# Kernel optimization log

Measured on AMD Instinct MI355X. Metric: run time of the kernel, lower is better.

The kernel has to match this reference:

```python
import jax, jax.numpy as jnp
import numpy as np

B, S, V, D, H, C, NH = 8, 512, 32000, 768, 768, 9, 8
DH = D // NH


def setup_inputs() -> dict:
    key = jax.random.key(0)
    ks = list(jax.random.split(key, 24))
    it = iter(ks)

    def w(shape, s=0.02):
        return jax.random.normal(next(it), shape, jnp.float32) * s

    return {
        "input_ids": jax.random.randint(next(it), (B, S), 0, V, dtype=jnp.int32),
        "labels": jax.random.randint(next(it), (B, S), 0, C, dtype=jnp.int32),
        "emb_table": w((V, D), 1.0),
        "hw_Wh": w((D, D)),
        "hw_bh": jnp.zeros((D,), jnp.float32),
        "hw_Wt": w((D, D)),
        "hw_bt": jnp.zeros((D,), jnp.float32),
        "in_proj_w": w((3 * D, D)),
        "in_proj_b": jnp.zeros((3 * D,), jnp.float32),
        "out_proj_w": w((D, D)),
        "out_proj_b": jnp.zeros((D,), jnp.float32),
        "lstm0_Wih": w((2, 4 * H, D)),
        "lstm0_Whh": w((2, 4 * H, H)),
        "lstm0_b": jnp.zeros((2, 4 * H), jnp.float32),
        "lstm1_Wih": w((2, 4 * H, 2 * H)),
        "lstm1_Whh": w((2, 4 * H, H)),
        "lstm1_b": jnp.zeros((2, 4 * H), jnp.float32),
        "fc_W": w((C, 2 * H)),
        "fc_b": jnp.zeros((C,), jnp.float32),
        "crf_start": w((C,), 0.1),
        "crf_end": w((C,), 0.1),
        "crf_trans": w((C, C), 0.1),
    }


def _lstm_dir(x, Wih, Whh, b, reverse):
    # x: [B,S,in] -> outputs [B,S,H]; PyTorch gate order i,f,g,o
    xt = x.transpose(1, 0, 2)  # [S,B,in]
    h0 = jnp.zeros((x.shape[0], H), x.dtype)

    def step(carry, xt_):
        h, c = carry
        g = xt_ @ Wih.T + h @ Whh.T + b
        i, f, gg, o = jnp.split(g, 4, axis=-1)
        c = jax.nn.sigmoid(f) * c + jax.nn.sigmoid(i) * jnp.tanh(gg)
        h = jax.nn.sigmoid(o) * jnp.tanh(c)
        return (h, c), h

    _, hs = jax.lax.scan(step, (h0, h0), xt, reverse=reverse)
    return hs.transpose(1, 0, 2)


def _bilstm_layer(x, Wih, Whh, b):
    fwd = _lstm_dir(x, Wih[0], Whh[0], b[0], False)
    bwd = _lstm_dir(x, Wih[1], Whh[1], b[1], True)
    return jnp.concatenate([fwd, bwd], axis=-1)


def _emissions(input_ids, emb_table, hw_Wh, hw_bh, hw_Wt, hw_bt,
               in_proj_w, in_proj_b, out_proj_w, out_proj_b,
               lstm0_Wih, lstm0_Whh, lstm0_b, lstm1_Wih, lstm1_Whh, lstm1_b,
               fc_W, fc_b):
    x = emb_table[input_ids]  # [B,S,D]
    # Highway (1 layer, relu)
    hh = jax.nn.relu(x @ hw_Wh.T + hw_bh)
    t = jax.nn.sigmoid(x @ hw_Wt.T + hw_bt)
    x = t * hh + (1.0 - t) * x
    # Multi-head self-attention
    qkv = x @ in_proj_w.T + in_proj_b
    q, k, v = jnp.split(qkv, 3, axis=-1)
    hd = lambda a: a.reshape(B, S, NH, DH).transpose(0, 2, 1, 3)  # [B,NH,S,DH]
    q, k, v = hd(q), hd(k), hd(v)
    att = jax.nn.softmax(jnp.einsum('bhqd,bhkd->bhqk', q, k) / np.float32(np.sqrt(DH)), axis=-1)
    o = jnp.einsum('bhqk,bhkd->bhqd', att, v).transpose(0, 2, 1, 3).reshape(B, S, D)
    x = o @ out_proj_w.T + out_proj_b
    # 2-layer BiLSTM (inference: dropout off)
    x = _bilstm_layer(x, lstm0_Wih, lstm0_Whh, lstm0_b)
    x = _bilstm_layer(x, lstm1_Wih, lstm1_Whh, lstm1_b)
    return x @ fc_W.T + fc_b  # [B,S,C]


def _crf_nll(emissions, tags, crf_start, crf_end, crf_trans):
    # full mask (labels==-100 replaced by 0 before mask built), reduction='sum'
    em_t = emissions.transpose(1, 0, 2)  # [S,B,C]
    num = crf_start[tags[:, 0]] + crf_end[tags[:, -1]]
    num = num + jnp.take_along_axis(emissions, tags[..., None], axis=-1)[..., 0].sum(-1)
    num = num + crf_trans[tags[:, :-1], tags[:, 1:]].sum(-1)
    a0 = crf_start + em_t[0]  # [B,C]

    def fstep(a, em):
        a = jax.scipy.special.logsumexp(a[:, :, None] + crf_trans[None], axis=1) + em
        return a, None

    aT, _ = jax.lax.scan(fstep, a0, em_t[1:])
    logZ = jax.scipy.special.logsumexp(aT + crf_end, axis=-1)
    return -(num - logZ).sum()


def _viterbi(emissions, crf_start, crf_end, crf_trans):
    em_t = emissions.transpose(1, 0, 2)  # [S,B,C]
    s0 = crf_start + em_t[0]

    def vstep(s, em):
        sc = s[:, :, None] + crf_trans[None]  # [B,C_prev,C_next]
        return jnp.max(sc, axis=1) + em, jnp.argmax(sc, axis=1)

    sT, bps = jax.lax.scan(vstep, s0, em_t[1:])  # bps: [S-1,B,C]
    last = jnp.argmax(sT + crf_end, axis=-1)  # [B]

    def bstep(tag, bp):
        prev = jnp.take_along_axis(bp, tag[:, None], axis=1)[:, 0]
        return prev, prev

    _, path = jax.lax.scan(bstep, last, bps, reverse=True)  # [S-1,B]
    return jnp.concatenate([path, last[None]], axis=0).transpose(1, 0)  # [B,S]


def reference(input_ids, labels, emb_table, hw_Wh, hw_bh, hw_Wt, hw_bt,
              in_proj_w, in_proj_b, out_proj_w, out_proj_b,
              lstm0_Wih, lstm0_Whh, lstm0_b, lstm1_Wih, lstm1_Whh, lstm1_b,
              fc_W, fc_b, crf_start, crf_end, crf_trans):
    emissions = _emissions(input_ids, emb_table, hw_Wh, hw_bh, hw_Wt, hw_bt,
                           in_proj_w, in_proj_b, out_proj_w, out_proj_b,
                           lstm0_Wih, lstm0_Whh, lstm0_b,
                           lstm1_Wih, lstm1_Whh, lstm1_b, fc_W, fc_b)
    loss = _crf_nll(emissions, labels, crf_start, crf_end, crf_trans)
    decode = _viterbi(emissions, crf_start, crf_end, crf_trans)
    return loss, decode
```

## Files before the change

### kernel.cpp

```cpp
#include <hip/hip_runtime.h>
#include <hip/hip_bf16.h>
#include <cstdint>

#define B_   8
#define S_   512
#define D_   768
#define C_   9
#define BS_  4096

typedef unsigned long long u64;
typedef unsigned short ushort_t;
typedef short bf16x8 __attribute__((ext_vector_type(8)));
typedef float f32x4 __attribute__((ext_vector_type(4)));

__global__ __launch_bounds__(192) void k_embed(const int* __restrict__ ids,
                                               const float* __restrict__ emb,
                                               float* __restrict__ x) {
  int row = blockIdx.x;
  int id = ids[row];
  const float4* src = (const float4*)(emb + (size_t)id * D_);
  float4* dst = (float4*)(x + (size_t)row * D_);
  dst[threadIdx.x] = src[threadIdx.x];
}

#define GIDX(k, m) ((k)*144 + (m) + (((m) >> 5) << 2))

__global__ __launch_bounds__(256) void k_gemm(const float* __restrict__ A,
                                              const float* __restrict__ W,
                                              const float* __restrict__ bias,
                                              float* __restrict__ C,
                                              int M, int N, int K, int act, int mode) {
  __shared__ float As[2304];
  __shared__ float Bs[2304];
  int nwg = gridDim.x * gridDim.y;
  int lin = blockIdx.y * gridDim.x + blockIdx.x;
  int cpx = nwg >> 3;
  int swz = (lin & 7) * cpx + (lin >> 3);
  int bxs = swz % gridDim.x, bys = swz / gridDim.x;
  int bm0 = bys * 128, bn0 = bxs * 128;
  int tid = threadIdx.x;
  int tm = tid >> 4, tn = tid & 15;
  float acc[8][8];
#pragma unroll
  for (int i = 0; i < 8; ++i)
#pragma unroll
    for (int j = 0; j < 8; ++j) acc[i][j] = 0.f;

  for (int k0 = 0; k0 < K; k0 += 16) {
    __syncthreads();
#pragma unroll
    for (int j = 0; j < 2; ++j) {
      int f4 = tid + j * 256;
      int r = f4 >> 2;
      int kq = (f4 & 3) * 4;
      float4 va = *(const float4*)(A + (size_t)(bm0 + r) * K + k0 + kq);
      As[GIDX(kq + 0, r)] = va.x; As[GIDX(kq + 1, r)] = va.y;
      As[GIDX(kq + 2, r)] = va.z; As[GIDX(kq + 3, r)] = va.w;
      float4 vb = *(const float4*)(W + (size_t)(bn0 + r) * K + k0 + kq);
      Bs[GIDX(kq + 0, r)] = vb.x; Bs[GIDX(kq + 1, r)] = vb.y;
      Bs[GIDX(kq + 2, r)] = vb.z; Bs[GIDX(kq + 3, r)] = vb.w;
    }
    __syncthreads();
#pragma unroll
    for (int kk = 0; kk < 16; ++kk) {
      float a[8], b[8];
      *(float4*)&a[0] = *(const float4*)&As[GIDX(kk, tm * 8)];
      *(float4*)&a[4] = *(const float4*)&As[GIDX(kk, tm * 8 + 4)];
      *(float4*)&b[0] = *(const float4*)&Bs[GIDX(kk, tn * 8)];
      *(float4*)&b[4] = *(const float4*)&Bs[GIDX(kk, tn * 8 + 4)];
#pragma unroll
      for (int i = 0; i < 8; ++i)
#pragma unroll
        for (int j = 0; j < 8; ++j) acc[i][j] += a[i] * b[j];
    }
  }

  float bv[8];
#pragma unroll
  for (int j = 0; j < 8; ++j) bv[j] = bias[bn0 + tn * 8 + j];
#pragma unroll
  for (int i = 0; i < 8; ++i) {
    int row = bm0 + tm * 8 + i;
    float o[8];
#pragma unroll
    for (int j = 0; j < 8; ++j) {
      float v = acc[i][j] + bv[j];
      if (act == 1) v = fmaxf(v, 0.f);
      else if (act == 2) v = 1.f / (1.f + expf(-v));
      o[j] = v;
    }
    if (mode == 0) {
      float* cp = C + (size_t)row * N + bn0 + tn * 8;
      *(float4*)cp = make_float4(o[0], o[1], o[2], o[3]);
      *(float4*)(cp + 4) = make_float4(o[4], o[5], o[6], o[7]);
    } else {
      int bb = row >> 9, t = row & 511;
#pragma unroll
      for (int j = 0; j < 8; ++j) {
        unsigned n = bn0 + tn * 8 + j;
        unsigned dir = n / 3072u;
        unsigned n2 = n - dir * 3072u;
        unsigned g = n2 / 768u;
        unsigned rem = n2 - g * 768u;
        unsigned grp = rem >> 3, u = rem & 7;
        C[(((size_t)(dir * 512 + t) * 96 + grp) << 8) + u * 32 + g * 8 + bb] = o[j];
      }
    }
  }
}

__device__ inline ushort_t f2bf_bits(float x) {
  __hip_bfloat16 h = __float2bfloat16(x);
  return __builtin_bit_cast(ushort_t, h);
}
__device__ inline float bf2f(ushort_t b) {
  return __bfloat162float(__builtin_bit_cast(__hip_bfloat16, b));
}

__global__ __launch_bounds__(256) void k_cvt(const float* __restrict__ src,
                                             ushort_t* __restrict__ dst,
                                             int K, int total4, int mode) {
  int kq4 = K >> 2;
  for (int idx = blockIdx.x * 256 + threadIdx.x; idx < total4; idx += gridDim.x * 256) {
    int m = idx / kq4;
    int kq = (idx - m * kq4) * 4;
    float4 v = *(const float4*)(src + (size_t)m * K + kq);
    ushort4 hi, lo;
    hi.x = f2bf_bits(v.x); lo.x = f2bf_bits(v.x - bf2f(hi.x));
    hi.y = f2bf_bits(v.y); lo.y = f2bf_bits(v.y - bf2f(hi.y));
    hi.z = f2bf_bits(v.z); lo.z = f2bf_bits(v.z - bf2f(hi.z));
    hi.w = f2bf_bits(v.w); lo.w = f2bf_bits(v.w - bf2f(hi.w));
    ushort_t* base = dst + (size_t)m * 3 * K + kq;
    *(ushort4*)(base)         = hi;
    *(ushort4*)(base + K)     = mode ? hi : lo;
    *(ushort4*)(base + 2 * K) = mode ? lo : hi;
  }
}

__global__ __launch_bounds__(256) void k_gates16(const ushort_t* __restrict__ A,
                                                 const ushort_t* __restrict__ W,
                                                 const float* __restrict__ bias,
                                                 float* __restrict__ C,
                                                 int Kp) {
  __shared__ ushort_t Asb[128 * 64];
  __shared__ ushort_t Bsb[128 * 64];
  int nwg = gridDim.x * gridDim.y;
  int lin = blockIdx.y * gridDim.x + blockIdx.x;
  int cpx = nwg >> 3;
  int swz = (lin & 7) * cpx + (lin >> 3);
  int bn0 = (swz % gridDim.x) * 128, bm0 = (swz / gridDim.x) * 128;
  int tid = threadIdx.x;
  int w = tid >> 6, lane = tid & 63;
  int lr = lane & 15, lq = lane >> 4;
  int srow = tid >> 1, shalf = tid & 1;

  f32x4 acc[2][8];
#pragma unroll
  for (int i = 0; i < 2; ++i)
#pragma unroll
    for (int j = 0; j < 8; ++j) acc[i][j] = (f32x4){0.f, 0.f, 0.f, 0.f};

  const ushort_t* Ap = A + (size_t)(bm0 + srow) * Kp + shalf * 32;
  const ushort_t* Wp = W + (size_t)(bn0 + srow) * Kp + shalf * 32;
  int s7 = srow & 7;

  for (int k0 = 0; k0 < Kp; k0 += 64) {
    __syncthreads();
#pragma unroll
    for (int i = 0; i < 4; ++i) {
      int c = shalf * 4 + i;
      int cs = c ^ s7;
      *(uint4*)&Asb[srow * 64 + cs * 8] = *(const uint4*)(Ap + k0 + i * 8);
      *(uint4*)&Bsb[srow * 64 + cs * 8] = *(const uint4*)(Wp + k0 + i * 8);
    }
    __syncthreads();
#pragma unroll
    for (int kf = 0; kf < 2; ++kf) {
      int c = kf * 4 + lq;
      int rowA0 = w * 32 + lr;
      int rowA1 = w * 32 + 16 + lr;
      bf16x8 a0 = *(const bf16x8*)&Asb[rowA0 * 64 + (c ^ (rowA0 & 7)) * 8];
      bf16x8 a1 = *(const bf16x8*)&Asb[rowA1 * 64 + (c ^ (rowA1 & 7)) * 8];
#pragma unroll
      for (int ns = 0; ns < 8; ++ns) {
        int rowB = ns * 16 + lr;
        bf16x8 b = *(const bf16x8*)&Bsb[rowB * 64 + (c ^ (rowB & 7)) * 8];
        acc[0][ns] = __builtin_amdgcn_mfma_f32_16x16x32_bf16(a0, b, acc[0][ns], 0, 0, 0);
        acc[1][ns] = __builtin_amdgcn_mfma_f32_16x16x32_bf16(a1, b, acc[1][ns], 0, 0, 0);
      }
    }
  }

#pragma unroll
  for (int ns = 0; ns < 8; ++ns) {
    unsigned n = bn0 + ns * 16 + lr;
    unsigned dir = n / 3072u;
    unsigned n2 = n - dir * 3072u;
    unsigned g = n2 / 768u;
    unsigned rem = n2 - g * 768u;
    unsigned grp = rem >> 3, u = rem & 7;
    float bv = bias[n];
#pragma unroll
    for (int ms = 0; ms < 2; ++ms) {
#pragma unroll
      for (int r = 0; r < 4; ++r) {
        int m = bm0 + w * 32 + ms * 16 + lq * 4 + r;
        int bb = m >> 9, t = m & 511;
        C[(((size_t)(dir * 512 + t) * 96 + grp) << 8) + u * 32 + g * 8 + bb] =
            acc[ms][ns][r] + bv;
      }
    }
  }
}

__global__ __launch_bounds__(256) void k_highway(float* __restrict__ x,
                                                 const float* __restrict__ hh,
                                                 const float* __restrict__ tt) {
  const int n4 = BS_ * D_ / 4;
  for (int i = blockIdx.x * 256 + threadIdx.x; i < n4; i += gridDim.x * 256) {
    float4 xv = ((const float4*)x)[i];
    float4 hv = ((const float4*)hh)[i];
    float4 tv = ((const float4*)tt)[i];
    xv.x = tv.x * hv.x + (1.f - tv.x) * xv.x;
    xv.y = tv.y * hv.y + (1.f - tv.y) * xv.y;
    xv.z = tv.z * hv.z + (1.f - tv.z) * xv.z;
    xv.w = tv.w * hv.w + (1.f - tv.w) * xv.w;
    ((float4*)x)[i] = xv;
  }
}

__global__ __launch_bounds__(256) void k_attn(const float* __restrict__ qkv,
                                              float* __restrict__ out) {
  __shared__ float Qs[16 * 100];
  __shared__ float Ks[32 * 101];
  __shared__ float Ps[16 * 513];
  int bh = blockIdx.x;
  int b = bh >> 3, h = bh & 7;
  int q0 = blockIdx.y * 16;
  int tid = threadIdx.x;
  const float scale = 0.10206207261596577f;

  const float* qb = qkv + (size_t)(b * 512 + q0) * 2304 + h * 96;
  for (int i = tid; i < 16 * 96; i += 256) {
    int r = i / 96, c = i - r * 96;
    Qs[r * 100 + c] = qb[(size_t)r * 2304 + c];
  }
  int qi = tid >> 4, kseg = tid & 15;

  for (int kt = 0; kt < 16; ++kt) {
    __syncthreads();
    const float* kb = qkv + (size_t)(b * 512 + kt * 32) * 2304 + 768 + h * 96;
    for (int i = tid; i < 32 * 96; i += 256) {
      int r = i / 96, c = i - r * 96;
      Ks[r * 101 + c] = kb[(size_t)r * 2304 + c];
    }
    __syncthreads();
    int kj0 = kseg * 2;
    float s0 = 0.f, s1 = 0.f;
    const float* qrow = &Qs[qi * 100];
    const float* k0p = &Ks[kj0 * 101];
    const float* k1p = &Ks[(kj0 + 1) * 101];
#pragma unroll 8
    for (int d = 0; d < 96; ++d) {
      float qv = qrow[d];
      s0 += qv * k0p[d];
      s1 += qv * k1p[d];
    }
    Ps[qi * 513 + kt * 32 + kj0] = s0 * scale;
    Ps[qi * 513 + kt * 32 + kj0 + 1] = s1 * scale;
  }
  __syncthreads();

  {
    float m = -1e30f;
    for (int j = 0; j < 32; ++j) m = fmaxf(m, Ps[qi * 513 + kseg + j * 16]);
    m = fmaxf(m, __shfl_xor(m, 1)); m = fmaxf(m, __shfl_xor(m, 2));
    m = fmaxf(m, __shfl_xor(m, 4)); m = fmaxf(m, __shfl_xor(m, 8));
    float sum = 0.f;
    for (int j = 0; j < 32; ++j) {
      int idx = qi * 513 + kseg + j * 16;
      float e = expf(Ps[idx] - m);
      Ps[idx] = e;
      sum += e;
    }
    sum += __shfl_xor(sum, 1); sum += __shfl_xor(sum, 2);
    sum += __shfl_xor(sum, 4); sum += __shfl_xor(sum, 8);
    float inv = 1.f / sum;
    for (int j = 0; j < 32; ++j) Ps[qi * 513 + kseg + j * 16] *= inv;
  }

  float acc[6] = {0.f, 0.f, 0.f, 0.f, 0.f, 0.f};
  int d0 = kseg * 6;
  for (int kt = 0; kt < 16; ++kt) {
    __syncthreads();
    const float* vb = qkv + (size_t)(b * 512 + kt * 32) * 2304 + 1536 + h * 96;
    for (int i = tid; i < 32 * 96; i += 256) {
      int r = i / 96, c = i - r * 96;
      Ks[r * 101 + c] = vb[(size_t)r * 2304 + c];
    }
    __syncthreads();
#pragma unroll 4
    for (int kj = 0; kj < 32; ++kj) {
      float p = Ps[qi * 513 + kt * 32 + kj];
      const float* vrow = &Ks[kj * 101 + d0];
#pragma unroll
      for (int u = 0; u < 6; ++u) acc[u] += p * vrow[u];
    }
  }
  float* ob = out + (size_t)(b * 512 + q0 + qi) * 768 + h * 96 + d0;
#pragma unroll
  for (int u = 0; u < 6; ++u) ob[u] = acc[u];
}

#define NWGD 96
__global__ __launch_bounds__(256, 1) void k_lstm(const float* __restrict__ gates,
                                                 const float* __restrict__ Whh,
                                                 float* __restrict__ hbuf,
                                                 float* __restrict__ hs,
                                                 int* __restrict__ flags) {
  __shared__ float hlds[8 * 772];
  int tid = threadIdx.x;
  int wg = blockIdx.x;
  int dir = wg / NWGD;
  int grp = wg % NWGD;
  int rg = tid >> 5;
  int ks = tid & 31;

  float4 w4[4][6];
#pragma unroll
  for (int j = 0; j < 4; ++j) {
    const float* wp = Whh + ((size_t)dir * 3072 + j * 768 + grp * 8 + rg) * 768 + ks * 4;
#pragma unroll
    for (int jj = 0; jj < 6; ++jj)
      w4[j][jj] = *(const float4*)(wp + jj * 128);
  }

  float* hb = hbuf + (size_t)dir * 2 * 6144;
  const float* gbase = gates + (size_t)dir * 512 * 24576 + grp * 256 + tid;
  const float* hp = hlds + ks * 4;
  float cst = 0.f;

  for (int step = 0; step < 512; ++step) {
    int t = dir ? (511 - step) : step;
    float gqv = gbase[(size_t)t * 24576];

#pragma unroll
    for (int i = 0; i < 3; ++i) {
      int idx = i * 256 + tid;
      int b2 = idx / 96;
      int kq = (idx - b2 * 96) * 8;
      const u64* src = (const u64*)(hb + (step & 1) * 6144 + b2 * 768 + kq);
      u64 lo  = __hip_atomic_load(src + 0, __ATOMIC_RELAXED, __HIP_MEMORY_SCOPE_AGENT);
      u64 hi  = __hip_atomic_load(src + 1, __ATOMIC_RELAXED, __HIP_MEMORY_SCOPE_AGENT);
      u64 lo2 = __hip_atomic_load(src + 2, __ATOMIC_RELAXED, __HIP_MEMORY_SCOPE_AGENT);
      u64 hi2 = __hip_atomic_load(src + 3, __ATOMIC_RELAXED, __HIP_MEMORY_SCOPE_AGENT);
      float* dst = &hlds[b2 * 772 + kq];
      *(u64*)(dst + 0) = lo;
      *(u64*)(dst + 2) = hi;
      *(u64*)(dst + 4) = lo2;
      *(u64*)(dst + 6) = hi2;
    }
    __syncthreads();

    float v[32];
#pragma unroll
    for (int i = 0; i < 32; ++i) v[i] = 0.f;
#pragma unroll
    for (int jj = 0; jj < 6; ++jj) {
#pragma unroll
      for (int b2 = 0; b2 < 8; ++b2) {
        float4 hv = *(const float4*)(hp + b2 * 772 + jj * 128);
#pragma unroll
        for (int j = 0; j < 4; ++j) {
          float4 w = w4[j][jj];
          v[j * 8 + b2] = fmaf(w.x, hv.x, v[j * 8 + b2]);
          v[j * 8 + b2] = fmaf(w.y, hv.y, v[j * 8 + b2]);
          v[j * 8 + b2] = fmaf(w.z, hv.z, v[j * 8 + b2]);
          v[j * 8 + b2] = fmaf(w.w, hv.w, v[j * 8 + b2]);
        }
      }
    }

    {
      bool hi = (ks & 16) != 0;
#pragma unroll
      for (int i = 0; i < 16; ++i) {
        float keep = hi ? v[i + 16] : v[i];
        float send = hi ? v[i] : v[i + 16];
        v[i] = keep + __shfl_xor(send, 16);
      }
    }
    {
      bool hi = (ks & 8) != 0;
#pragma unroll
      for (int i = 0; i < 8; ++i) {
        float keep = hi ? v[i + 8] : v[i];
        float send = hi ? v[i] : v[i + 8];
        v[i] = keep + __shfl_xor(send, 8);
      }
    }
    {
      bool hi = (ks & 4) != 0;
#pragma unroll
      for (int i = 0; i < 4; ++i) {
        float keep = hi ? v[i + 4] : v[i];
        float send = hi ? v[i] : v[i + 4];
        v[i] = keep + __shfl_xor(send, 4);
      }
    }
    {
      bool hi = (ks & 2) != 0;
#pragma unroll
      for (int i = 0; i < 2; ++i) {
        float keep = hi ? v[i + 2] : v[i];
        float send = hi ? v[i] : v[i + 2];
        v[i] = keep + __shfl_xor(send, 2);
      }
    }
    {
      bool hi = (ks & 1) != 0;
      float keep = hi ? v[1] : v[0];
      float send = hi ? v[0] : v[1];
      v[0] = keep + __shfl_xor(send, 1);
    }

    float gv = v[0] + gqv;
    float gf = __shfl_down(gv, 8);
    float gg = __shfl_down(gv, 16);
    float go = __shfl_down(gv, 24);
    float hnew = 0.f;
    if (ks < 8) {
      float i_ = 1.f / (1.f + expf(-gv));
      float f_ = 1.f / (1.f + expf(-gf));
      float ci = tanhf(gg);
      float o_ = 1.f / (1.f + expf(-go));
      cst = f_ * cst + i_ * ci;
      hnew = o_ * tanhf(cst);
      __hip_atomic_store(hb + (size_t)((step + 1) & 1) * 6144 + ks * 768 + grp * 8 + rg,
                         hnew, __ATOMIC_RELAXED, __HIP_MEMORY_SCOPE_AGENT);
    }

    __syncthreads();
    if (tid == 0)
      __hip_atomic_store(&flags[wg * 32], step + 1, __ATOMIC_RELAXED, __HIP_MEMORY_SCOPE_AGENT);
    if (ks < 8)
      hs[((size_t)(ks * 512 + t)) * 1536 + dir * 768 + grp * 8 + rg] = hnew;
    if (tid < NWGD) {
      const int* fp = &flags[(dir * NWGD + tid) * 32];
      while (__hip_atomic_load(fp, __ATOMIC_RELAXED, __HIP_MEMORY_SCOPE_AGENT) <= step)
        __builtin_amdgcn_s_sleep(2);
    }
    __syncthreads();
  }
}

__global__ __launch_bounds__(256) void k_fc(const float* __restrict__ A,
                                            const float* __restrict__ Wf,
                                            const float* __restrict__ bf,
                                            float* __restrict__ out) {
  __shared__ float Wl[9 * 1536];
  int tid = threadIdx.x;
  for (int i = tid; i < 9 * 1536; i += 256) Wl[i] = Wf[i];
  __syncthreads();
  int lane = tid & 63, wv = tid >> 6;
  int row = blockIdx.x * 4 + wv;
  const float* a = A + (size_t)row * 1536;
  float acc[9];
#pragma unroll
  for (int c = 0; c < 9; ++c) acc[c] = 0.f;
  for (int i = 0; i < 24; ++i) {
    float av = a[lane + i * 64];
#pragma unroll
    for (int c = 0; c < 9; ++c) acc[c] += av * Wl[c * 1536 + lane + i * 64];
  }
#pragma unroll
  for (int c = 0; c < 9; ++c) {
#pragma unroll
    for (int m = 1; m < 64; m <<= 1) acc[c] += __shfl_xor(acc[c], m);
  }
  if (lane == 0) {
#pragma unroll
    for (int c = 0; c < 9; ++c) out[(size_t)row * 9 + c] = acc[c] + bf[c];
  }
}

__global__ __launch_bounds__(512) void k_crf(const float* __restrict__ em,
                                             const int* __restrict__ labels,
                                             const float* __restrict__ cs,
                                             const float* __restrict__ ce,
                                             const float* __restrict__ ct,
                                             float* __restrict__ out) {
  __shared__ float trans_s[81];
  __shared__ unsigned char bps[8][511][12];
  __shared__ float partres[16];
  int tid = threadIdx.x;
  int b = tid >> 6;
  int lane = tid & 63;
  bool act = lane < 9;
  if (tid < 81) trans_s[tid] = ct[tid];
  __syncthreads();

  float tcol[9];
#pragma unroll
  for (int cp = 0; cp < 9; ++cp) tcol[cp] = act ? trans_s[cp * 9 + lane] : 0.f;

  float a_ = -1e30f, v_ = -1e30f;
  if (act) {
    float e0 = em[((size_t)b * 512) * 9 + lane];
    a_ = cs[lane] + e0;
    v_ = a_;
  }

  float e = act ? em[((size_t)b * 512 + 1) * 9 + lane] : 0.f;
  for (int t = 1; t < 512; ++t) {
    float e_nxt = 0.f;
    if (act && t < 511) e_nxt = em[((size_t)b * 512 + t + 1) * 9 + lane];
    float m = -1e30f, vm = -1e30f;
    int bp = 0;
    float xs[9];
#pragma unroll
    for (int cp = 0; cp < 9; ++cp) {
      float ap = __shfl(a_, cp);
      float vp = __shfl(v_, cp);
      float x = ap + tcol[cp];
      xs[cp] = x;
      m = fmaxf(m, x);
      float y = vp + tcol[cp];
      if (y > vm) { vm = y; bp = cp; }
    }
    float ssum = 0.f;
#pragma unroll
    for (int cp = 0; cp < 9; ++cp) ssum += expf(xs[cp] - m);
    if (act) {
      a_ = m + logf(ssum) + e;
      v_ = vm + e;
      bps[b][t - 1][lane] = (unsigned char)bp;
    }
    e = e_nxt;
  }

  float fin = act ? a_ + ce[lane] : -1e30f;
  float vfin = act ? v_ + ce[lane] : -1e30f;
  float m2 = fin;
  m2 = fmaxf(m2, __shfl_xor(m2, 1)); m2 = fmaxf(m2, __shfl_xor(m2, 2));
  m2 = fmaxf(m2, __shfl_xor(m2, 4)); m2 = fmaxf(m2, __shfl_xor(m2, 8));
  float s2 = expf(fin - m2);
  s2 += __shfl_xor(s2, 1); s2 += __shfl_xor(s2, 2);
  s2 += __shfl_xor(s2, 4); s2 += __shfl_xor(s2, 8);
  float logZ = m2 + logf(s2);

  float bv = vfin; int bi = lane;
#pragma unroll
  for (int s = 1; s < 16; s <<= 1) {
    float ov = __shfl_xor(bv, s);
    int oi = __shfl_xor(bi, s);
    if (ov > bv || (ov == bv && oi < bi)) { bv = ov; bi = oi; }
  }

  float np = 0.f;
  for (int t = lane; t < 512; t += 64) {
    int tg = labels[b * 512 + t];
    np += em[((size_t)b * 512 + t) * 9 + tg];
    if (t < 511) np += trans_s[tg * 9 + labels[b * 512 + t + 1]];
  }
#pragma unroll
  for (int s = 1; s < 64; s <<= 1) np += __shfl_xor(np, s);

  if (lane == 0) {
    np += cs[labels[b * 512]] + ce[labels[b * 512 + 511]];
    partres[b] = np;
    partres[8 + b] = logZ;
    out[1 + b * 512 + 511] = (float)bi;
    int tg = bi;
    for (int t = 510; t >= 0; --t) {
      tg = bps[b][t][tg];
      out[1 + b * 512 + t] = (float)tg;
    }
  }
  __syncthreads();
  if (tid == 0) {
    float acc = 0.f;
#pragma unroll
    for (int b2 = 0; b2 < 8; ++b2) acc += partres[b2] - partres[8 + b2];
    out[0] = -acc;
  }
}

extern "C" void kernel_launch(void* const* d_in, const int* in_sizes, int n_in,
                              void* d_out, int out_size, void* d_ws, size_t ws_size,
                              hipStream_t stream) {
  (void)in_sizes; (void)n_in; (void)out_size;
  const int*   ids    = (const int*)d_in[0];
  const int*   labels = (const int*)d_in[1];
  const float* emb    = (const float*)d_in[2];
  const float* hwWh   = (const float*)d_in[3];
  const float* hwbh   = (const float*)d_in[4];
  const float* hwWt   = (const float*)d_in[5];
  const float* hwbt   = (const float*)d_in[6];
  const float* ipw    = (const float*)d_in[7];
  const float* ipb    = (const float*)d_in[8];
  const float* opw    = (const float*)d_in[9];
  const float* opb    = (const float*)d_in[10];
  const float* l0Wih  = (const float*)d_in[11];
  const float* l0Whh  = (const float*)d_in[12];
  const float* l0b    = (const float*)d_in[13];
  const float* l1Wih  = (const float*)d_in[14];
  const float* l1Whh  = (const float*)d_in[15];
  const float* l1b    = (const float*)d_in[16];
  const float* fcW    = (const float*)d_in[17];
  const float* fcb    = (const float*)d_in[18];
  const float* cs     = (const float*)d_in[19];
  const float* ce     = (const float*)d_in[20];
  const float* ct     = (const float*)d_in[21];

  float* ws   = (float*)d_ws;
  float* x0   = ws;
  float* gbuf = ws + 3145728;
  float* hh   = gbuf;
  float* tt   = gbuf + 3145728;
  float* qkv  = gbuf + 6291456;
  float* x1   = ws + 28311552;
  float* hs0  = ws + 31457280;
  float* hs1  = ws + 37748736;
  float* em   = ws + 44040192;
  float* hbuf = ws + 44077056;
  int*   flags = (int*)(ws + 44101632);
  ushort_t* bfA = (ushort_t*)(ws + 44107776);
  ushort_t* bfW = (ushort_t*)(ws + 44107776 + 9437184);
  const size_t ws_need = (44107776ull + 9437184ull + 14155776ull) * 4ull;
  bool bf16path = (ws_size >= ws_need);

  dim3 g768(6, 32), g2304(18, 32), g6144(48, 32);

  k_embed<<<BS_, 192, 0, stream>>>(ids, emb, x0);
  k_gemm<<<g768, 256, 0, stream>>>(x0, hwWh, hwbh, hh, BS_, 768, 768, 1, 0);
  k_gemm<<<g768, 256, 0, stream>>>(x0, hwWt, hwbt, tt, BS_, 768, 768, 2, 0);
  k_highway<<<768, 256, 0, stream>>>(x0, hh, tt);
  k_gemm<<<g2304, 256, 0, stream>>>(x0, ipw, ipb, qkv, BS_, 2304, 768, 0, 0);
  k_attn<<<dim3(64, 32), 256, 0, stream>>>(qkv, x0);
  k_gemm<<<g768, 256, 0, stream>>>(x0, opw, opb, x1, BS_, 768, 768, 0, 0);

  if (bf16path) {
    k_cvt<<<2048, 256, 0, stream>>>(x1, bfA, 768, BS_ * 768 / 4, 0);
    k_cvt<<<2048, 256, 0, stream>>>(l0Wih, bfW, 768, 6144 * 768 / 4, 1);
    k_gates16<<<g6144, 256, 0, stream>>>(bfA, bfW, l0b, gbuf, 2304);
  } else {
    k_gemm<<<g6144, 256, 0, stream>>>(x1, l0Wih, l0b, gbuf, BS_, 6144, 768, 0, 1);
  }
  hipMemsetAsync(hbuf, 0, (24576 + 192 * 32) * sizeof(float), stream);
  k_lstm<<<192, 256, 0, stream>>>(gbuf, l0Whh, hbuf, hs0, flags);

  if (bf16path) {
    k_cvt<<<2048, 256, 0, stream>>>(hs0, bfA, 1536, BS_ * 1536 / 4, 0);
    k_cvt<<<4096, 256, 0, stream>>>(l1Wih, bfW, 1536, 6144 * 1536 / 4, 1);
    k_gates16<<<g6144, 256, 0, stream>>>(bfA, bfW, l1b, gbuf, 4608);
  } else {
    k_gemm<<<g6144, 256, 0, stream>>>(hs0, l1Wih, l1b, gbuf, BS_, 6144, 1536, 0, 1);
  }
  hipMemsetAsync(hbuf, 0, (24576 + 192 * 32) * sizeof(float), stream);
  k_lstm<<<192, 256, 0, stream>>>(gbuf, l1Whh, hbuf, hs1, flags);

  k_fc<<<1024, 256, 0, stream>>>(hs1, fcW, fcb, em);
  k_crf<<<1, 512, 0, stream>>>(em, labels, cs, ce, ct, (float*)d_out);
}
```

Baseline: 7.465 ms.

## Route highway, QKV and out-proj GEMMs through split-bf16 MFMA with direct LDS loads

Generalizes the bf16 MFMA gate kernel into k_mfma, which adds a row-major epilogue with optional relu or sigmoid activation. The four pre-LSTM projections (highway H and T, QKV in-projection, out-projection) now use the split hi/lo bf16 triple-K MFMA path instead of the fp32 k_gemm. The shared-memory tile fill switches from register-staged uint4 copies to global_load_lds direct-to-LDS transfers. This moves the small GEMMs onto matrix cores, at the cost of extra conversion kernels for activations and weights on every call.

```diff
diff --git a/kernel.cpp b/kernel.cpp
--- a/kernel.cpp
+++ b/kernel.cpp
@@ -12,6 +12,8 @@
 typedef unsigned short ushort_t;
 typedef short bf16x8 __attribute__((ext_vector_type(8)));
 typedef float f32x4 __attribute__((ext_vector_type(4)));
+typedef __attribute__((address_space(1))) const void gvoid_t;
+typedef __attribute__((address_space(3))) void svoid_t;
 
 __global__ __launch_bounds__(192) void k_embed(const int* __restrict__ ids,
                                                const float* __restrict__ emb,
@@ -137,11 +139,11 @@
   }
 }
 
-__global__ __launch_bounds__(256) void k_gates16(const ushort_t* __restrict__ A,
-                                                 const ushort_t* __restrict__ W,
-                                                 const float* __restrict__ bias,
-                                                 float* __restrict__ C,
-                                                 int Kp) {
+__global__ __launch_bounds__(256) void k_mfma(const ushort_t* __restrict__ A,
+                                              const ushort_t* __restrict__ W,
+                                              const float* __restrict__ bias,
+                                              float* __restrict__ C,
+                                              int N, int Kp, int act, int mode) {
   __shared__ ushort_t Asb[128 * 64];
   __shared__ ushort_t Bsb[128 * 64];
   int nwg = gridDim.x * gridDim.y;
@@ -152,7 +154,6 @@
   int tid = threadIdx.x;
   int w = tid >> 6, lane = tid & 63;
   int lr = lane & 15, lq = lane >> 4;
-  int srow = tid >> 1, shalf = tid & 1;
 
   f32x4 acc[2][8];
 #pragma unroll
@@ -160,54 +161,76 @@
 #pragma unroll
     for (int j = 0; j < 8; ++j) acc[i][j] = (f32x4){0.f, 0.f, 0.f, 0.f};
 
-  const ushort_t* Ap = A + (size_t)(bm0 + srow) * Kp + shalf * 32;
-  const ushort_t* Wp = W + (size_t)(bn0 + srow) * Kp + shalf * 32;
-  int s7 = srow & 7;
+  int srow0 = tid >> 3;
+  int sc = tid & 7;
 
   for (int k0 = 0; k0 < Kp; k0 += 64) {
     __syncthreads();
 #pragma unroll
-    for (int i = 0; i < 4; ++i) {
-      int c = shalf * 4 + i;
-      int cs = c ^ s7;
-      *(uint4*)&Asb[srow * 64 + cs * 8] = *(const uint4*)(Ap + k0 + i * 8);
-      *(uint4*)&Bsb[srow * 64 + cs * 8] = *(const uint4*)(Wp + k0 + i * 8);
+    for (int it = 0; it < 4; ++it) {
+      int row = it * 32 + srow0;
+      int soff = (sc ^ (row & 7)) * 8;
+      const ushort_t* ga = A + (size_t)(bm0 + row) * Kp + k0 + soff;
+      const ushort_t* gb = W + (size_t)(bn0 + row) * Kp + k0 + soff;
+      char* la = (char*)Asb + it * 4096 + (tid & 192) * 16;
+      char* lb = (char*)Bsb + it * 4096 + (tid & 192) * 16;
+      __builtin_amdgcn_global_load_lds((gvoid_t*)ga, (svoid_t*)la, 16, 0, 0);
+      __builtin_amdgcn_global_load_lds((gvoid_t*)gb, (svoid_t*)lb, 16, 0, 0);
     }
     __syncthreads();
 #pragma unroll
     for (int kf = 0; kf < 2; ++kf) {
       int c = kf * 4 + lq;
       int rowA0 = w * 32 + lr;
-      int rowA1 = w * 32 + 16 + lr;
-      bf16x8 a0 = *(const bf16x8*)&Asb[rowA0 * 64 + (c ^ (rowA0 & 7)) * 8];
-      bf16x8 a1 = *(const bf16x8*)&Asb[rowA1 * 64 + (c ^ (rowA1 & 7)) * 8];
+      int rowA1 = rowA0 + 16;
+      bf16x8 a0 = *(const bf16x8*)&Asb[rowA0 * 64 + ((c ^ (rowA0 & 7)) << 3)];
+      bf16x8 a1 = *(const bf16x8*)&Asb[rowA1 * 64 + ((c ^ (rowA1 & 7)) << 3)];
 #pragma unroll
       for (int ns = 0; ns < 8; ++ns) {
         int rowB = ns * 16 + lr;
-        bf16x8 b = *(const bf16x8*)&Bsb[rowB * 64 + (c ^ (rowB & 7)) * 8];
+        bf16x8 b = *(const bf16x8*)&Bsb[rowB * 64 + ((c ^ (rowB & 7)) << 3)];
         acc[0][ns] = __builtin_amdgcn_mfma_f32_16x16x32_bf16(a0, b, acc[0][ns], 0, 0, 0);
         acc[1][ns] = __builtin_amdgcn_mfma_f32_16x16x32_bf16(a1, b, acc[1][ns], 0, 0, 0);
       }
     }
   }
 
-#pragma unroll
-  for (int ns = 0; ns < 8; ++ns) {
-    unsigned n = bn0 + ns * 16 + lr;
-    unsigned dir = n / 3072u;
-    unsigned n2 = n - dir * 3072u;
-    unsigned g = n2 / 768u;
-    unsigned rem = n2 - g * 768u;
-    unsigned grp = rem >> 3, u = rem & 7;
-    float bv = bias[n];
-#pragma unroll
-    for (int ms = 0; ms < 2; ++ms) {
-#pragma unroll
-      for (int r = 0; r < 4; ++r) {
-        int m = bm0 + w * 32 + ms * 16 + lq * 4 + r;
-        int bb = m >> 9, t = m & 511;
-        C[(((size_t)(dir * 512 + t) * 96 + grp) << 8) + u * 32 + g * 8 + bb] =
-            acc[ms][ns][r] + bv;
+  if (mode == 1) {
+#pragma unroll
+    for (int ns = 0; ns < 8; ++ns) {
+      unsigned n = bn0 + ns * 16 + lr;
+      unsigned dir = n / 3072u;
+      unsigned n2 = n - dir * 3072u;
+      unsigned g = n2 / 768u;
+      unsigned rem = n2 - g * 768u;
+      unsigned grp = rem >> 3, u = rem & 7;
+      float bv = bias[n];
+#pragma unroll
+      for (int ms = 0; ms < 2; ++ms) {
+#pragma unroll
+        for (int r = 0; r < 4; ++r) {
+          int m = bm0 + w * 32 + ms * 16 + lq * 4 + r;
+          int bb = m >> 9, t = m & 511;
+          C[(((size_t)(dir * 512 + t) * 96 + grp) << 8) + u * 32 + g * 8 + bb] =
+              acc[ms][ns][r] + bv;
+        }
+      }
+    }
+  } else {
+#pragma unroll
+    for (int ns = 0; ns < 8; ++ns) {
+      int col = bn0 + ns * 16 + lr;
+      float bv = bias[col];
+#pragma unroll
+      for (int ms = 0; ms < 2; ++ms) {
+#pragma unroll
+        for (int r = 0; r < 4; ++r) {
+          int m = bm0 + w * 32 + ms * 16 + lq * 4 + r;
+          float v = acc[ms][ns][r] + bv;
+          if (act == 1) v = fmaxf(v, 0.f);
+          else if (act == 2) v = 1.f / (1.f + expf(-v));
+          C[(size_t)m * N + col] = v;
+        }
       }
     }
   }
@@ -633,18 +656,31 @@
   dim3 g768(6, 32), g2304(18, 32), g6144(48, 32);
 
   k_embed<<<BS_, 192, 0, stream>>>(ids, emb, x0);
-  k_gemm<<<g768, 256, 0, stream>>>(x0, hwWh, hwbh, hh, BS_, 768, 768, 1, 0);
-  k_gemm<<<g768, 256, 0, stream>>>(x0, hwWt, hwbt, tt, BS_, 768, 768, 2, 0);
-  k_highway<<<768, 256, 0, stream>>>(x0, hh, tt);
-  k_gemm<<<g2304, 256, 0, stream>>>(x0, ipw, ipb, qkv, BS_, 2304, 768, 0, 0);
-  k_attn<<<dim3(64, 32), 256, 0, stream>>>(qkv, x0);
-  k_gemm<<<g768, 256, 0, stream>>>(x0, opw, opb, x1, BS_, 768, 768, 0, 0);
 
   if (bf16path) {
+    k_cvt<<<2048, 256, 0, stream>>>(x0, bfA, 768, BS_ * 768 / 4, 0);
+    k_cvt<<<2048, 256, 0, stream>>>(hwWh, bfW, 768, 768 * 768 / 4, 1);
+    k_mfma<<<g768, 256, 0, stream>>>(bfA, bfW, hwbh, hh, 768, 2304, 1, 0);
+    k_cvt<<<2048, 256, 0, stream>>>(hwWt, bfW, 768, 768 * 768 / 4, 1);
+    k_mfma<<<g768, 256, 0, stream>>>(bfA, bfW, hwbt, tt, 768, 2304, 2, 0);
+    k_highway<<<768, 256, 0, stream>>>(x0, hh, tt);
+    k_cvt<<<2048, 256, 0, stream>>>(x0, bfA, 768, BS_ * 768 / 4, 0);
+    k_cvt<<<2048, 256, 0, stream>>>(ipw, bfW, 768, 2304 * 768 / 4, 1);
+    k_mfma<<<g2304, 256, 0, stream>>>(bfA, bfW, ipb, qkv, 2304, 2304, 0, 0);
+    k_attn<<<dim3(64, 32), 256, 0, stream>>>(qkv, x0);
+    k_cvt<<<2048, 256, 0, stream>>>(x0, bfA, 768, BS_ * 768 / 4, 0);
+    k_cvt<<<2048, 256, 0, stream>>>(opw, bfW, 768, 768 * 768 / 4, 1);
+    k_mfma<<<g768, 256, 0, stream>>>(bfA, bfW, opb, x1, 768, 2304, 0, 0);
     k_cvt<<<2048, 256, 0, stream>>>(x1, bfA, 768, BS_ * 768 / 4, 0);
     k_cvt<<<2048, 256, 0, stream>>>(l0Wih, bfW, 768, 6144 * 768 / 4, 1);
-    k_gates16<<<g6144, 256, 0, stream>>>(bfA, bfW, l0b, gbuf, 2304);
+    k_mfma<<<g6144, 256, 0, stream>>>(bfA, bfW, l0b, gbuf, 6144, 2304, 0, 1);
   } else {
+    k_gemm<<<g768, 256, 0, stream>>>(x0, hwWh, hwbh, hh, BS_, 768, 768, 1, 0);
+    k_gemm<<<g768, 256, 0, stream>>>(x0, hwWt, hwbt, tt, BS_, 768, 768, 2, 0);
+    k_highway<<<768, 256, 0, stream>>>(x0, hh, tt);
+    k_gemm<<<g2304, 256, 0, stream>>>(x0, ipw, ipb, qkv, BS_, 2304, 768, 0, 0);
+    k_attn<<<dim3(64, 32), 256, 0, stream>>>(qkv, x0);
+    k_gemm<<<g768, 256, 0, stream>>>(x0, opw, opb, x1, BS_, 768, 768, 0, 0);
     k_gemm<<<g6144, 256, 0, stream>>>(x1, l0Wih, l0b, gbuf, BS_, 6144, 768, 0, 1);
   }
   hipMemsetAsync(hbuf, 0, (24576 + 192 * 32) * sizeof(float), stream);
@@ -653,7 +689,7 @@
   if (bf16path) {
     k_cvt<<<2048, 256, 0, stream>>>(hs0, bfA, 1536, BS_ * 1536 / 4, 0);
     k_cvt<<<4096, 256, 0, stream>>>(l1Wih, bfW, 1536, 6144 * 1536 / 4, 1);
-    k_gates16<<<g6144, 256, 0, stream>>>(bfA, bfW, l1b, gbuf, 4608);
+    k_mfma<<<g6144, 256, 0, stream>>>(bfA, bfW, l1b, gbuf, 6144, 4608, 0, 1);
   } else {
     k_gemm<<<g6144, 256, 0, stream>>>(hs0, l1Wih, l1b, gbuf, BS_, 6144, 1536, 0, 1);
   }
```

New measurement: 7.186 ms, median of 2. 1.04x faster.
